# Kernel tuning notes

Hardware: AMD Instinct MI355X
Metric: run time of the kernel (lower is better)

The kernel has to match this reference:

```python
import jax, jax.numpy as jnp
import numpy as np

O, C_IN, P, D = 256, 256, 96, 2
KH, KW = 51, 51


def setup_inputs() -> dict:
    key = jax.random.key(0)
    k1, k2, k3 = jax.random.split(key, 3)
    # coordinate grid in [-1, 1], shape (1, D, KH, KW) like a normalized meshgrid
    ys = jnp.linspace(-1.0, 1.0, KH, dtype=jnp.float32)
    xs = jnp.linspace(-1.0, 1.0, KW, dtype=jnp.float32)
    gy, gx = jnp.meshgrid(ys, xs, indexing="ij")
    x = jnp.stack([gy, gx], axis=0)[None]  # (1, 2, KH, KW)
    # learned point coordinates, trunc-normal-ish in [-1, 1]
    weight_coord = jnp.clip(0.3 * jax.random.normal(k1, (O, P, D), dtype=jnp.float32), -1.0, 1.0)
    # per-point radius, initialized to init_radius
    radius = jnp.full((O, P, 1, 1), 0.5, dtype=jnp.float32)
    # point weights
    weights = 0.02 * jax.random.normal(k2, (O, C_IN, P), dtype=jnp.float32)
    return {"x": x, "weight_coord": weight_coord, "radius": radius, "weights": weights}


def reference(x, weight_coord, radius, weights):
    o, p, d = weight_coord.shape
    spatial = x.shape[2:]  # (KH, KW)
    n = int(np.prod(spatial))
    coords = x.reshape(d, n).T  # (N, D)
    # broadcast coord diff + L1 distance over dim_linear: (O, P, N)
    dist = jnp.sum(jnp.abs(weight_coord[:, :, None, :] - coords[None, None, :, :]), axis=-1)
    # triangular basis
    vals = jax.nn.relu(1.0 - dist / radius.reshape(o, p, 1))  # (O, P, N)
    # count of points covering each location, used to normalize
    count = jnp.sum(vals != 0, axis=1, keepdims=True)  # (O, 1, N), int
    weighted = vals / (count.astype(vals.dtype) + 1e-6)
    # batched small matmul over points: (O, C_in, P) @ (O, P, N) -> (O, C_in, N)
    kernels = jnp.einsum("ocp,opn->ocn", weights, weighted)
    kernels = kernels.reshape(o, weights.shape[1], *spatial)
    # dim_linear == 2 branch: transpose last two dims, flip along dim 2
    kernels = jnp.flip(jnp.swapaxes(kernels, -2, -1), axis=2)
    return kernels
```

## Files before the change

### kernel.cpp

```cpp
#include <hip/hip_runtime.h>

#define O_DIM 256
#define C_DIM 256
#define P_DIM 96
#define KHW 51
#define NSP 2601
#define RPITCH 1044
#define PHW 1024

typedef __attribute__((ext_vector_type(8))) short short8v;
typedef __attribute__((ext_vector_type(4))) float float4v;
typedef __attribute__((ext_vector_type(4), aligned(16))) float float4a;
typedef __attribute__((ext_vector_type(4), aligned(4))) float float4u;

static __device__ __forceinline__ unsigned f2bf(float f) {
  union { float f; unsigned u; } v; v.f = f;
  return (v.u + 0x7FFFu + ((v.u >> 16) & 1u)) >> 16;
}
static __device__ __forceinline__ unsigned cvtpk(float lo, float hi) {
  unsigned r;
  asm("v_cvt_pk_bf16_f32 %0, %1, %2" : "=v"(r) : "v"(lo), "v"(hi));
  return r;
}
static __device__ __forceinline__ float bcast(unsigned u) {
  union { unsigned u; float f; } v; v.u = u; return v.f;
}
static __device__ __forceinline__ void barrier_lgkm() {
  asm volatile("s_waitcnt lgkmcnt(0)" ::: "memory");
  __builtin_amdgcn_s_barrier();
}

__global__ __launch_bounds__(1024, 1) void smp_fused(
    const float* __restrict__ xg,
    const float* __restrict__ wc,
    const float* __restrict__ rad,
    const float* __restrict__ wts,
    float* __restrict__ out)
{
  __shared__ float Ylds[52];
  __shared__ __align__(16) float pyL[96], pxL[96], prL[96];
  __shared__ __align__(16) unsigned short RBuf[64 * RPITCH];

  const int b = blockIdx.x;
  const int o = b >> 2;
  const int cq = b & 3;
  const int tid = threadIdx.x;
  const int wave = tid >> 6;
  const int lane = tid & 63;
  const int row16 = lane & 15;
  const int kgrp = lane >> 4;

  if (tid < 51) Ylds[tid] = xg[tid * KHW];
  if (tid < 96) {
    pyL[tid] = wc[((size_t)o * P_DIM + tid) * 2];
    pxL[tid] = wc[((size_t)o * P_DIM + tid) * 2 + 1];
    prL[tid] = 1.0f / rad[(size_t)o * P_DIM + tid];
  }

  short8v wfr[4][3];
  {
    const float* Wo = wts + ((size_t)o * C_DIM + cq * 64) * P_DIM;
#pragma unroll
    for (int mf = 0; mf < 4; ++mf) {
      const float* src = Wo + (mf * 16 + row16) * P_DIM;
#pragma unroll
      for (int ks = 0; ks < 3; ++ks) {
        const float4 a4 = *(const float4*)(src + ks * 32 + kgrp * 8);
        const float4 c4 = *(const float4*)(src + ks * 32 + kgrp * 8 + 4);
        short8v f;
        f[0] = (short)f2bf(a4.x); f[1] = (short)f2bf(a4.y);
        f[2] = (short)f2bf(a4.z); f[3] = (short)f2bf(a4.w);
        f[4] = (short)f2bf(c4.x); f[5] = (short)f2bf(c4.y);
        f[6] = (short)f2bf(c4.z); f[7] = (short)f2bf(c4.w);
        wfr[mf][ks] = f;
      }
    }
  }
  __syncthreads();

  const size_t obase = ((size_t)o * C_DIM + cq * 64) * NSP;

  for (int p = 0; p < 3; ++p) {
    const int base = p * PHW;
    const int width = (p < 2) ? PHW : (NSP - 2 * PHW);
    const int ntiles = (p < 2) ? 64 : 35;

    for (int t = wave; t < ntiles; t += 16) {
      const int jlc = t * 16 + row16;
      const int jl = base + jlc;
      const int jc = jl < NSP ? jl : NSP - 1;
      const int i = jc / KHW;
      const int jj = jc - i * KHW;
      const float gy = Ylds[jj];
      const float gx = Ylds[50 - i];

      float4v acc[4];
#pragma unroll
      for (int mf = 0; mf < 4; ++mf) acc[mf] = (float4v){0.f, 0.f, 0.f, 0.f};
      int cnt = 0;

#pragma unroll
      for (int ks = 0; ks < 3; ++ks) {
        const int pb = ks * 32 + kgrp * 8;
        const float4a py0 = *(const float4a*)&pyL[pb];
        const float4a py1 = *(const float4a*)&pyL[pb + 4];
        const float4a px0 = *(const float4a*)&pxL[pb];
        const float4a px1 = *(const float4a*)&pxL[pb + 4];
        const float4a pr0 = *(const float4a*)&prL[pb];
        const float4a pr1 = *(const float4a*)&prL[pb + 4];
        float s[8], v[8];
#pragma unroll
        for (int j = 0; j < 4; ++j) {
          s[j]     = fmaf(fabsf(py0[j] - gy) + fabsf(px0[j] - gx), -pr0[j], 1.0f);
          s[j + 4] = fmaf(fabsf(py1[j] - gy) + fabsf(px1[j] - gx), -pr1[j], 1.0f);
        }
#pragma unroll
        for (int j = 0; j < 8; ++j) {
          v[j] = s[j] > 0.0f ? s[j] : 0.0f;
          cnt += (s[j] > 0.0f);
        }
        union { unsigned u[4]; short8v sv; } bfr;
#pragma unroll
        for (int jp = 0; jp < 4; ++jp) bfr.u[jp] = cvtpk(v[2 * jp], v[2 * jp + 1]);
#pragma unroll
        for (int mf = 0; mf < 4; ++mf)
          acc[mf] = __builtin_amdgcn_mfma_f32_16x16x32_bf16(
              wfr[mf][ks], bfr.sv, acc[mf], 0, 0, 0);
      }
      cnt += __shfl_xor(cnt, 16);
      cnt += __shfl_xor(cnt, 32);
      const float inv = __builtin_amdgcn_rcpf((float)cnt + 1e-6f);

      if (jl < NSP) {
#pragma unroll
        for (int mf = 0; mf < 4; ++mf)
#pragma unroll
          for (int r2 = 0; r2 < 4; ++r2)
            RBuf[(mf * 16 + kgrp * 4 + r2) * RPITCH + jlc] =
                (unsigned short)f2bf(acc[mf][r2] * inv);
      }
    }
    barrier_lgkm();

#pragma unroll
    for (int k2 = 0; k2 < 4; ++k2) {
      const int row = wave + k2 * 16;
      const unsigned short* rb = &RBuf[row * RPITCH];
      float* gp = out + obase + (size_t)row * NSP + base;
      for (int it = 0; it < width / 256; ++it) {
        const int j = it * 256 + lane * 4;
        const uint2 u = *(const uint2*)&rb[j];
        float4u v = {bcast(u.x << 16), bcast(u.x & 0xFFFF0000u),
                     bcast(u.y << 16), bcast(u.y & 0xFFFF0000u)};
        *(float4u*)(gp + j) = v;
      }
      if (width & 255) {
        const int j = (width & ~255) + lane * 4;
        if (j + 4 <= width) {
          const uint2 u = *(const uint2*)&rb[j];
          float4u v = {bcast(u.x << 16), bcast(u.x & 0xFFFF0000u),
                       bcast(u.y << 16), bcast(u.y & 0xFFFF0000u)};
          *(float4u*)(gp + j) = v;
        } else if (j < width) {
#pragma unroll
          for (int r2 = 0; r2 < 4; ++r2)
            if (j + r2 < width) gp[j + r2] = bcast(((unsigned)rb[j + r2]) << 16);
        }
      }
    }
    barrier_lgkm();
  }
}

extern "C" void kernel_launch(void* const* d_in, const int* in_sizes, int n_in,
                              void* d_out, int out_size, void* d_ws, size_t ws_size,
                              hipStream_t stream) {
  const float* xg  = (const float*)d_in[0];
  const float* wcp = (const float*)d_in[1];
  const float* rad = (const float*)d_in[2];
  const float* wts = (const float*)d_in[3];
  float* out = (float*)d_out;
  hipLaunchKernelGGL(smp_fused, dim3(O_DIM * 4), dim3(1024), 0, stream,
                     xg, wcp, rad, wts, out);
}
```

Before: 230.4 us.

## Use smaller blocks with double-buffered 256-column LDS slabs and one barrier

Each block now processes the 2601 output columns in eleven 256-wide slabs instead of three 1024-wide passes. The LDS staging buffer is double-buffered, so the barrier after the global store phase is dropped. Blocks shrink from 1024 to 512 threads with a launch bound allowing several blocks per CU, so MFMA compute and global writes from different blocks and slabs can overlap. The cost is more slab iterations and barriers per block, and achieved occupancy depends on the roughly 68KB of LDS each block still uses.

```diff
diff --git a/kernel.cpp b/kernel.cpp
--- a/kernel.cpp
+++ b/kernel.cpp
@@ -5,8 +5,9 @@
 #define P_DIM 96
 #define KHW 51
 #define NSP 2601
-#define RPITCH 1044
-#define PHW 1024
+#define SLAB 256
+#define NSLAB 11
+#define RP2 268
 
 typedef __attribute__((ext_vector_type(8))) short short8v;
 typedef __attribute__((ext_vector_type(4))) float float4v;
@@ -30,7 +31,7 @@
   __builtin_amdgcn_s_barrier();
 }
 
-__global__ __launch_bounds__(1024, 1) void smp_fused(
+__global__ __launch_bounds__(512, 4) void smp_fused(
     const float* __restrict__ xg,
     const float* __restrict__ wc,
     const float* __restrict__ rad,
@@ -39,7 +40,7 @@
 {
   __shared__ float Ylds[52];
   __shared__ __align__(16) float pyL[96], pxL[96], prL[96];
-  __shared__ __align__(16) unsigned short RBuf[64 * RPITCH];
+  __shared__ __align__(16) unsigned short RBuf[2][64 * RP2];
 
   const int b = blockIdx.x;
   const int o = b >> 2;
@@ -80,12 +81,13 @@
 
   const size_t obase = ((size_t)o * C_DIM + cq * 64) * NSP;
 
-  for (int p = 0; p < 3; ++p) {
-    const int base = p * PHW;
-    const int width = (p < 2) ? PHW : (NSP - 2 * PHW);
-    const int ntiles = (p < 2) ? 64 : 35;
+  for (int s = 0; s < NSLAB; ++s) {
+    const int base = s * SLAB;
+    const int width = (s < NSLAB - 1) ? SLAB : (NSP - (NSLAB - 1) * SLAB);
+    const int ntiles = (width + 15) >> 4;
+    unsigned short* rb = &RBuf[s & 1][0];
 
-    for (int t = wave; t < ntiles; t += 16) {
+    for (int t = wave; t < ntiles; t += 8) {
       const int jlc = t * 16 + row16;
       const int jl = base + jlc;
       const int jc = jl < NSP ? jl : NSP - 1;
@@ -108,16 +110,16 @@
         const float4a px1 = *(const float4a*)&pxL[pb + 4];
         const float4a pr0 = *(const float4a*)&prL[pb];
         const float4a pr1 = *(const float4a*)&prL[pb + 4];
-        float s[8], v[8];
+        float sx[8], v[8];
 #pragma unroll
         for (int j = 0; j < 4; ++j) {
-          s[j]     = fmaf(fabsf(py0[j] - gy) + fabsf(px0[j] - gx), -pr0[j], 1.0f);
-          s[j + 4] = fmaf(fabsf(py1[j] - gy) + fabsf(px1[j] - gx), -pr1[j], 1.0f);
+          sx[j]     = fmaf(fabsf(py0[j] - gy) + fabsf(px0[j] - gx), -pr0[j], 1.0f);
+          sx[j + 4] = fmaf(fabsf(py1[j] - gy) + fabsf(px1[j] - gx), -pr1[j], 1.0f);
         }
 #pragma unroll
         for (int j = 0; j < 8; ++j) {
-          v[j] = s[j] > 0.0f ? s[j] : 0.0f;
-          cnt += (s[j] > 0.0f);
+          v[j] = sx[j] > 0.0f ? sx[j] : 0.0f;
+          cnt += (sx[j] > 0.0f);
         }
         union { unsigned u[4]; short8v sv; } bfr;
 #pragma unroll
@@ -131,44 +133,46 @@
       cnt += __shfl_xor(cnt, 32);
       const float inv = __builtin_amdgcn_rcpf((float)cnt + 1e-6f);
 
-      if (jl < NSP) {
 #pragma unroll
-        for (int mf = 0; mf < 4; ++mf)
+      for (int mf = 0; mf < 4; ++mf)
 #pragma unroll
-          for (int r2 = 0; r2 < 4; ++r2)
-            RBuf[(mf * 16 + kgrp * 4 + r2) * RPITCH + jlc] =
-                (unsigned short)f2bf(acc[mf][r2] * inv);
-      }
+        for (int r2 = 0; r2 < 4; ++r2)
+          rb[(mf * 16 + kgrp * 4 + r2) * RP2 + jlc] =
+              (unsigned short)f2bf(acc[mf][r2] * inv);
     }
     barrier_lgkm();
 
+    if (width == SLAB) {
 #pragma unroll
-    for (int k2 = 0; k2 < 4; ++k2) {
-      const int row = wave + k2 * 16;
-      const unsigned short* rb = &RBuf[row * RPITCH];
-      float* gp = out + obase + (size_t)row * NSP + base;
-      for (int it = 0; it < width / 256; ++it) {
-        const int j = it * 256 + lane * 4;
-        const uint2 u = *(const uint2*)&rb[j];
+      for (int k2 = 0; k2 < 8; ++k2) {
+        const int row = wave + k2 * 8;
+        const unsigned short* rr = &rb[row * RP2];
+        float* gp = out + obase + (size_t)row * NSP + base;
+        const int j = lane * 4;
+        const uint2 u = *(const uint2*)&rr[j];
         float4u v = {bcast(u.x << 16), bcast(u.x & 0xFFFF0000u),
                      bcast(u.y << 16), bcast(u.y & 0xFFFF0000u)};
         *(float4u*)(gp + j) = v;
       }
-      if (width & 255) {
-        const int j = (width & ~255) + lane * 4;
+    } else {
+#pragma unroll
+      for (int k2 = 0; k2 < 8; ++k2) {
+        const int row = wave + k2 * 8;
+        const unsigned short* rr = &rb[row * RP2];
+        float* gp = out + obase + (size_t)row * NSP + base;
+        const int j = lane * 4;
         if (j + 4 <= width) {
-          const uint2 u = *(const uint2*)&rb[j];
+          const uint2 u = *(const uint2*)&rr[j];
           float4u v = {bcast(u.x << 16), bcast(u.x & 0xFFFF0000u),
                        bcast(u.y << 16), bcast(u.y & 0xFFFF0000u)};
           *(float4u*)(gp + j) = v;
         } else if (j < width) {
 #pragma unroll
           for (int r2 = 0; r2 < 4; ++r2)
-            if (j + r2 < width) gp[j + r2] = bcast(((unsigned)rb[j + r2]) << 16);
+            if (j + r2 < width) gp[j + r2] = bcast(((unsigned)rr[j + r2]) << 16);
         }
       }
     }
-    barrier_lgkm();
   }
 }
 
@@ -180,6 +184,6 @@
   const float* rad = (const float*)d_in[2];
   const float* wts = (const float*)d_in[3];
   float* out = (float*)d_out;
-  hipLaunchKernelGGL(smp_fused, dim3(O_DIM * 4), dim3(1024), 0, stream,
+  hipLaunchKernelGGL(smp_fused, dim3(O_DIM * 4), dim3(512), 0, stream,
                      xg, wcp, rad, wts, out);
 }
```

After: 355.3 us. +54.2%, slower.
